# Optimization experiments

Hardware: AMD Instinct MI355X
Metric: run time of the kernel (lower is better)

Reference implementation:

```python
import jax, jax.numpy as jnp
import numpy as np

N, FEAT, D, K, L, H, NCLS = 4096, 512, 64, 100, 3, 8, 2
EPS = 1e-15

def _ln(x, g, b, eps=1e-6):
    m = x.mean(-1, keepdims=True)
    v = x.var(-1, keepdims=True)
    return (x - m) * jax.lax.rsqrt(v + eps) * g + b


def setup_inputs():
    key = jax.random.key(0)
    ks = jax.random.split(key, 12)
    w = lambda k, shape: jax.random.normal(k, shape, jnp.float32) * 0.02
    return {
        "node_feat": jax.random.normal(ks[0], (1, N, FEAT), jnp.float32),
        "adj": jax.random.uniform(ks[1], (1, N, N), jnp.float32),
        "conv_w": w(ks[2], (FEAT, D)), "conv_b": jnp.zeros((D,), jnp.float32),
        "bn_g": jnp.ones((D,), jnp.float32), "bn_b": jnp.zeros((D,), jnp.float32),
        "pool_w": w(ks[3], (D, K)), "pool_b": jnp.zeros((K,), jnp.float32),
        "cls_token": jnp.zeros((1, 1, D), jnp.float32),
        "ln1_g": jnp.ones((L, D), jnp.float32), "ln1_b": jnp.zeros((L, D), jnp.float32),
        "qkv_w": w(ks[4], (L, D, 3 * D)), "qkv_b": jnp.zeros((L, 3 * D), jnp.float32),
        "proj_w": w(ks[5], (L, D, D)), "proj_b": jnp.zeros((L, D), jnp.float32),
        "ln2_g": jnp.ones((L, D), jnp.float32), "ln2_b": jnp.zeros((L, D), jnp.float32),
        "fc1_w": w(ks[6], (L, D, 4 * D)), "fc1_b": jnp.zeros((L, 4 * D), jnp.float32),
        "fc2_w": w(ks[7], (L, 4 * D, D)), "fc2_b": jnp.zeros((L, D), jnp.float32),
        "norm_g": jnp.ones((D,), jnp.float32), "norm_b": jnp.zeros((D,), jnp.float32),
        "head_w": w(ks[8], (D, NCLS)), "head_b": jnp.zeros((NCLS,), jnp.float32),
    }


def _forward(node_feat, adj, conv_w, conv_b, bn_g, bn_b, pool_w, pool_b, cls_token,
             ln1_g, ln1_b, qkv_w, qkv_b, proj_w, proj_b, ln2_g, ln2_b,
             fc1_w, fc1_b, fc2_w, fc2_b, norm_g, norm_b, head_w, head_b):
    x = node_feat  # mask is all ones -> X = mask*X is a no-op
    # --- GCNBlock: propagate + self loop + linear + BatchNorm(train stats) + L2 norm ---
    y = jnp.matmul(adj, x) + x                 # [1,N,F]
    y = y @ conv_w + conv_b                    # [1,N,D]
    m = y.mean(axis=(0, 1))
    v = y.var(axis=(0, 1))
    y = (y - m) * jax.lax.rsqrt(v + 1e-5) * bn_g + bn_b
    y = y / jnp.maximum(jnp.linalg.norm(y, axis=2, keepdims=True), 1e-12)
    # --- cluster assignment ---
    s = jax.nn.softmax(y @ pool_w + pool_b, axis=-1)   # [1,N,K]
    # --- dense_mincut_pool ---
    out = jnp.einsum('bnk,bnd->bkd', s, y)             # [1,K,D]
    sa = s[0].T @ adj[0]                               # [K,N] (the torch.sparse.mm)
    out_adj = (sa @ s[0])[None]                        # [1,K,K]
    mincut_num = jnp.trace(out_adj, axis1=1, axis2=2)  # [1]
    d_flat = adj.sum(-1)                               # [1,N] degrees
    # trace(S^T diag(d) S) = sum_i d_i * ||s_i||^2
    mincut_den = jnp.sum(d_flat[0] * jnp.sum(s[0] ** 2, axis=-1))[None]
    mincut_loss = jnp.mean(-(mincut_num / mincut_den))
    ss = jnp.einsum('bnk,bnl->bkl', s, s)
    i_s = jnp.eye(K, dtype=ss.dtype)
    ortho_loss = jnp.mean(jnp.linalg.norm(
        ss / jnp.linalg.norm(ss, axis=(-1, -2), keepdims=True) - i_s / jnp.linalg.norm(i_s),
        axis=(-1, -2)))
    ind = jnp.arange(K)
    out_adj = out_adj.at[:, ind, ind].set(0.0)
    dd = jnp.sqrt(out_adj.sum(-1))[:, None] + EPS      # [1,1,K]
    out_adj = out_adj / dd / jnp.swapaxes(dd, 1, 2)    # (returned by pool; unused downstream)
    # --- transformer over [cls] + K cluster tokens ---
    t = jnp.concatenate([jnp.broadcast_to(cls_token, (1, 1, D)), out], axis=1)  # [1,K+1,D]
    hd = D // H
    scale = hd ** -0.5
    for l in range(L):
        h = _ln(t, ln1_g[l], ln1_b[l])
        qkv = h @ qkv_w[l] + qkv_b[l]
        q, k, vv = jnp.split(qkv, 3, axis=-1)
        sp = lambda a: a.reshape(1, -1, H, hd).transpose(0, 2, 1, 3)
        q, k, vv = sp(q), sp(k), sp(vv)
        att = jax.nn.softmax(jnp.einsum('bhqd,bhkd->bhqk', q, k) * scale, axis=-1)
        o = jnp.einsum('bhqk,bhkd->bhqd', att, vv).transpose(0, 2, 1, 3).reshape(1, -1, D)
        t = t + (o @ proj_w[l] + proj_b[l])
        h = _ln(t, ln2_g[l], ln2_b[l])
        t = t + (jax.nn.gelu(h @ fc1_w[l] + fc1_b[l], approximate=False) @ fc2_w[l] + fc2_b[l])
    t = _ln(t, norm_g, norm_b)
    logits = t[:, 0] @ head_w + head_b                 # [1,NCLS]
    return logits, mincut_loss, ortho_loss


def reference(node_feat, adj, conv_w, conv_b, bn_g, bn_b, pool_w, pool_b, cls_token,
              ln1_g, ln1_b, qkv_w, qkv_b, proj_w, proj_b, ln2_g, ln2_b,
              fc1_w, fc1_b, fc2_w, fc2_b, norm_g, norm_b, head_w, head_b):
    return _forward(node_feat, adj, conv_w, conv_b, bn_g, bn_b, pool_w, pool_b, cls_token,
                    ln1_g, ln1_b, qkv_w, qkv_b, proj_w, proj_b, ln2_g, ln2_b,
                    fc1_w, fc1_b, fc2_w, fc2_b, norm_g, norm_b, head_w, head_b)
```

## Files before the change

### kernel.cpp

```cpp
#include <hip/hip_runtime.h>
#include <hip/hip_bf16.h>
#include <math.h>

#define NN   4096
#define FEAT 512
#define DIM  64
#define KC   100
#define LL   3

#define OFF_DFLAT   0
#define OFF_CHSUM   4096
#define OFF_CHSQ    4160
#define ZERO_FLOATS 4224
#define OFF_XW      4224
#define OFF_XWPART  (OFF_XW + NN*DIM)
#define OFF_GPART   OFF_XWPART
#define OFF_YPART   (OFF_XWPART + 8*NN*DIM)
#define OFF_Y0      (OFF_YPART + 8*NN*DIM)
#define OFF_TBUF    (OFF_Y0 + NN*DIM)
#define OFF_QKV     (OFF_TBUF + 101*DIM)
#define OFF_SS      (OFF_QKV + 101*192)
#define OFF_DENP    (OFF_SS + KC*KC)
#define OFF_NUMP    (OFF_DENP + 1024)
#define OFF_SB16    (OFF_NUMP + 1024)
#define OFF_STB16   (OFF_SB16 + NN*128/2)
#define OFF_YNT16   (OFF_STB16 + NN*128/2)
#define OFF_XWT16   (OFF_YNT16 + NN*DIM/2)

typedef __attribute__((ext_vector_type(8))) short bfrag;
typedef __attribute__((ext_vector_type(4))) float ffrag;

__device__ __forceinline__ unsigned short f2bf(float f) {
    union { float f; unsigned u; } v; v.f = f;
    return (unsigned short)((v.u + 0x7FFFu + ((v.u >> 16) & 1u)) >> 16);
}
__device__ __forceinline__ float bf2f(unsigned short u) {
    union { unsigned u; float f; } v; v.u = (unsigned)u << 16; return v.f;
}
__device__ __forceinline__ unsigned int pk2(float a, float b) {
    __hip_bfloat162 h = __float22bfloat162_rn(make_float2(a, b));
    return *(unsigned int*)&h;
}

__device__ __forceinline__ float wsum(float v) {
#pragma unroll
    for (int o = 32; o > 0; o >>= 1) v += __shfl_xor(v, o, 64);
    return v;
}
__device__ __forceinline__ float wmax(float v) {
#pragma unroll
    for (int o = 32; o > 0; o >>= 1) v = fmaxf(v, __shfl_xor(v, o, 64));
    return v;
}
__device__ __forceinline__ float hsum32(float v) {
#pragma unroll
    for (int o = 16; o > 0; o >>= 1) v += __shfl_xor(v, o, 64);
    return v;
}
__device__ __forceinline__ float hmax32(float v) {
#pragma unroll
    for (int o = 16; o > 0; o >>= 1) v = fmaxf(v, __shfl_xor(v, o, 64));
    return v;
}

template<int KDIM>
__global__ __launch_bounds__(256) void mm64(const float* __restrict__ A,
                                            const float* __restrict__ B,
                                            float* __restrict__ outp) {
    __shared__ float a_sh[64 * 68];
    __shared__ float b_sh[64 * 68];
    const int t  = threadIdx.x;
    const int rb = blockIdx.x;
    const int kspan = KDIM / gridDim.y;
    const int k0 = blockIdx.y * kspan;
    const int cg = t & 15, rg = t >> 4;
    const int srow = t >> 2, sq = t & 3;
    float4 acc[4];
#pragma unroll
    for (int i = 0; i < 4; ++i) acc[i] = make_float4(0.f, 0.f, 0.f, 0.f);
    const float* arow = A + (size_t)(rb * 64 + srow) * KDIM + k0;
    const float* brow = B + (size_t)(k0 + srow) * DIM;
    for (int kt = 0; kt < kspan; kt += 64) {
#pragma unroll
        for (int k = 0; k < 4; ++k) {
            const int j = sq * 4 + 16 * k;
            *(float4*)&a_sh[srow * 68 + j] = *(const float4*)(arow + kt + j);
            *(float4*)&b_sh[srow * 68 + j] = *(const float4*)(brow + (size_t)kt * DIM + j);
        }
        __syncthreads();
#pragma unroll 4
        for (int jj = 0; jj < 64; jj += 4) {
            const float4 w0 = *(float4*)&b_sh[(jj + 0) * 68 + 4 * cg];
            const float4 w1 = *(float4*)&b_sh[(jj + 1) * 68 + 4 * cg];
            const float4 w2 = *(float4*)&b_sh[(jj + 2) * 68 + 4 * cg];
            const float4 w3 = *(float4*)&b_sh[(jj + 3) * 68 + 4 * cg];
#pragma unroll
            for (int i = 0; i < 4; ++i) {
                const float4 av = *(float4*)&a_sh[(4 * rg + i) * 68 + jj];
                acc[i].x += av.x * w0.x + av.y * w1.x + av.z * w2.x + av.w * w3.x;
                acc[i].y += av.x * w0.y + av.y * w1.y + av.z * w2.y + av.w * w3.y;
                acc[i].z += av.x * w0.z + av.y * w1.z + av.z * w2.z + av.w * w3.z;
                acc[i].w += av.x * w0.w + av.y * w1.w + av.z * w2.w + av.w * w3.w;
            }
        }
        __syncthreads();
    }
    const int M = gridDim.x * 64;
    float* op = outp + (size_t)blockIdx.y * M * DIM;
#pragma unroll
    for (int i = 0; i < 4; ++i)
        *(float4*)&op[(size_t)(rb * 64 + 4 * rg + i) * DIM + 4 * cg] = acc[i];
}

__global__ __launch_bounds__(256) void xwred2(const float* __restrict__ part,
                                              float* __restrict__ xw,
                                              unsigned short* __restrict__ xwT) {
    __shared__ unsigned short tl[64 * 17];
    const int t = threadIdx.x, b = blockIdx.x;
    const int nb = t >> 4, d0 = (t & 15) * 4;
    const size_t e = ((size_t)(b * 16 + nb)) * 64 + d0;
    float4 v = *(const float4*)(part + e);
#pragma unroll
    for (int s = 1; s < 8; ++s) {
        const float4 u = *(const float4*)(part + (size_t)s * NN * DIM + e);
        v.x += u.x; v.y += u.y; v.z += u.z; v.w += u.w;
    }
    *(float4*)(xw + e) = v;
    tl[(d0 + 0) * 17 + nb] = f2bf(v.x);
    tl[(d0 + 1) * 17 + nb] = f2bf(v.y);
    tl[(d0 + 2) * 17 + nb] = f2bf(v.z);
    tl[(d0 + 3) * 17 + nb] = f2bf(v.w);
    __syncthreads();
    const int d = t >> 2, c = (t & 3) * 4;
    ushort4 o;
    o.x = tl[d * 17 + c + 0]; o.y = tl[d * 17 + c + 1];
    o.z = tl[d * 17 + c + 2]; o.w = tl[d * 17 + c + 3];
    *(ushort4*)(xwT + (size_t)d * NN + b * 16 + c) = o;
}

__global__ __launch_bounds__(256) void gemmA(const float* __restrict__ adj,
                                             const unsigned short* __restrict__ xwT,
                                             float* __restrict__ ypart,
                                             float* __restrict__ dflat) {
    __shared__ __align__(16) unsigned short a_sh[32 * 72];
    __shared__ __align__(16) unsigned short b_sh[64 * 72];
    const int t  = threadIdx.x;
    const int rb = blockIdx.x;
    const int k0 = blockIdx.y * 512;
    const int w = t >> 6, lane = t & 63;
    const int m = lane & 15, q = lane >> 4;
    const int ih = w & 1, jh = w >> 1;
    const int srow = t >> 3, sq = t & 7;
    const int bn = t >> 2, bc = t & 3;
    ffrag acc[2];
    acc[0] = (ffrag){0.f, 0.f, 0.f, 0.f};
    acc[1] = (ffrag){0.f, 0.f, 0.f, 0.f};
    float dacc = 0.f;
    const float* abase = adj + (size_t)(rb * 32 + srow) * NN + k0;
    const unsigned short* bbase = xwT + (size_t)bn * NN + k0;
    for (int kt = 0; kt < 512; kt += 64) {
#pragma unroll
        for (int k = 0; k < 2; ++k) {
            const int p = sq + 8 * k;
            const float4 v = *(const float4*)(abase + kt + 4 * p);
            dacc += v.x + v.y + v.z + v.w;
            *(uint2*)(a_sh + srow * 72 + 4 * p) = make_uint2(pk2(v.x, v.y), pk2(v.z, v.w));
        }
#pragma unroll
        for (int k = 0; k < 2; ++k) {
            const int c2 = bc + 4 * k;
            *(bfrag*)(b_sh + bn * 72 + c2 * 8) = *(const bfrag*)(bbase + kt + c2 * 8);
        }
        __syncthreads();
#pragma unroll
        for (int ks = 0; ks < 2; ++ks) {
            const bfrag af = *(const bfrag*)(a_sh + (ih * 16 + m) * 72 + ks * 32 + q * 8);
#pragma unroll
            for (int jj = 0; jj < 2; ++jj) {
                const bfrag bf = *(const bfrag*)(b_sh + ((jh * 2 + jj) * 16 + m) * 72 + ks * 32 + q * 8);
                acc[jj] = __builtin_amdgcn_mfma_f32_16x16x32_bf16(af, bf, acc[jj], 0, 0, 0);
            }
        }
        __syncthreads();
    }
    float* op = ypart + (size_t)blockIdx.y * NN * DIM;
#pragma unroll
    for (int jj = 0; jj < 2; ++jj)
#pragma unroll
        for (int r = 0; r < 4; ++r)
            op[(size_t)(rb * 32 + ih * 16 + q * 4 + r) * DIM + jh * 32 + jj * 16 + m] = acc[jj][r];
    dacc += __shfl_down(dacc, 1, 64);
    dacc += __shfl_down(dacc, 2, 64);
    dacc += __shfl_down(dacc, 4, 64);
    if (sq == 0) atomicAdd(&dflat[rb * 32 + srow], dacc);
}

__global__ __launch_bounds__(256) void spmmT(const float* __restrict__ adj,
                                             const unsigned short* __restrict__ ST,
                                             const unsigned short* __restrict__ Sb16,
                                             float* __restrict__ nump) {
    __shared__ __align__(16) unsigned short a_sh[32 * 72];
    __shared__ __align__(16) unsigned short s_sh[128 * 72];
    __shared__ float red[4];
    const int t  = threadIdx.x;
    const int rb = blockIdx.x;
    const int k0 = blockIdx.y * 512;
    const int w = t >> 6, lane = t & 63;
    const int m = lane & 15, q = lane >> 4;
    const int rh = w & 1, ch = w >> 1;
    const int srow = t >> 3, sq = t & 7;
    const int sn = t >> 1, sc = t & 1;
    ffrag acc[4];
#pragma unroll
    for (int j = 0; j < 4; ++j) acc[j] = (ffrag){0.f, 0.f, 0.f, 0.f};
    const float* abase = adj + (size_t)(rb * 32 + srow) * NN + k0;
    const unsigned short* sbase = ST + (size_t)sn * NN + k0;
    for (int kt = 0; kt < 512; kt += 64) {
#pragma unroll
        for (int k = 0; k < 2; ++k) {
            const int p = sq + 8 * k;
            const float4 v = *(const float4*)(abase + kt + 4 * p);
            *(uint2*)(a_sh + srow * 72 + 4 * p) = make_uint2(pk2(v.x, v.y), pk2(v.z, v.w));
        }
#pragma unroll
        for (int k = 0; k < 4; ++k) {
            const int c2 = sc + 2 * k;
            *(bfrag*)(s_sh + sn * 72 + c2 * 8) = *(const bfrag*)(sbase + kt + c2 * 8);
        }
        __syncthreads();
#pragma unroll
        for (int ks = 0; ks < 2; ++ks) {
            const bfrag af = *(const bfrag*)(a_sh + (rh * 16 + m) * 72 + ks * 32 + q * 8);
#pragma unroll
            for (int j = 0; j < 4; ++j) {
                const bfrag bf = *(const bfrag*)(s_sh + ((ch * 4 + j) * 16 + m) * 72 + ks * 32 + q * 8);
                acc[j] = __builtin_amdgcn_mfma_f32_16x16x32_bf16(af, bf, acc[j], 0, 0, 0);
            }
        }
        __syncthreads();
    }
    float local = 0.f;
#pragma unroll
    for (int j = 0; j < 4; ++j)
#pragma unroll
        for (int r = 0; r < 4; ++r) {
            const int row = rb * 32 + rh * 16 + q * 4 + r;
            const int col = ch * 64 + j * 16 + m;
            local += acc[j][r] * bf2f(Sb16[(size_t)row * 128 + col]);
        }
    local = wsum(local);
    if (lane == 0) red[w] = local;
    __syncthreads();
    if (t == 0) nump[blockIdx.y * 128 + blockIdx.x] = red[0] + red[1] + red[2] + red[3];
}

__global__ __launch_bounds__(256) void bnstat(const float* __restrict__ ypart,
                                              const float* __restrict__ xw,
                                              const float* __restrict__ conv_b,
                                              float* __restrict__ Y0,
                                              float* __restrict__ chsum,
                                              float* __restrict__ chsq) {
    __shared__ float ssum[64], ssq[64];
    const int t = threadIdx.x;
    if (t < 64) { ssum[t] = 0.f; ssq[t] = 0.f; }
    __syncthreads();
    const int tid = blockIdx.x * 256 + t;
    const size_t e = (size_t)tid * 4;
    const int c0 = (int)(e & 63);
    float4 v = *(const float4*)(xw + e);
#pragma unroll
    for (int s = 0; s < 8; ++s) {
        const float4 u = *(const float4*)(ypart + (size_t)s * NN * DIM + e);
        v.x += u.x; v.y += u.y; v.z += u.z; v.w += u.w;
    }
    const float4 b = *(const float4*)(conv_b + c0);
    v.x += b.x; v.y += b.y; v.z += b.z; v.w += b.w;
    *(float4*)(Y0 + e) = v;
    atomicAdd(&ssum[c0 + 0], v.x); atomicAdd(&ssum[c0 + 1], v.y);
    atomicAdd(&ssum[c0 + 2], v.z); atomicAdd(&ssum[c0 + 3], v.w);
    atomicAdd(&ssq[c0 + 0], v.x * v.x); atomicAdd(&ssq[c0 + 1], v.y * v.y);
    atomicAdd(&ssq[c0 + 2], v.z * v.z); atomicAdd(&ssq[c0 + 3], v.w * v.w);
    __syncthreads();
    if (t < 64) { atomicAdd(&chsum[t], ssum[t]); atomicAdd(&chsq[t], ssq[t]); }
}

__global__ __launch_bounds__(256) void rowsk(const float* __restrict__ Y0,
                                             const float* __restrict__ bn_g,
                                             const float* __restrict__ bn_b,
                                             const float* __restrict__ chsum,
                                             const float* __restrict__ chsq,
                                             const float* __restrict__ pool_w,
                                             const float* __restrict__ pool_b,
                                             const float* __restrict__ dflat,
                                             unsigned short* __restrict__ YnT,
                                             unsigned short* __restrict__ Sb16,
                                             float* __restrict__ denp) {
    __shared__ float scale_sh[64], shift_sh[64];
    __shared__ float yn_sh[4][64];
    __shared__ float4 pw4[16 * 104];
    __shared__ float denw[4];
    const int t = threadIdx.x;
    if (t < 64) {
        const float mn  = chsum[t] * (1.f / 4096.f);
        const float var = chsq[t] * (1.f / 4096.f) - mn * mn;
        const float sc  = bn_g[t] * rsqrtf(var + 1e-5f);
        scale_sh[t] = sc;
        shift_sh[t] = bn_b[t] - mn * sc;
    }
    for (int idx = t; idx < 16 * KC; idx += 256) {
        const int dq = idx / KC, k = idx - dq * KC;
        pw4[dq * 104 + k] = make_float4(pool_w[(4 * dq + 0) * KC + k],
                                        pool_w[(4 * dq + 1) * KC + k],
                                        pool_w[(4 * dq + 2) * KC + k],
                                        pool_w[(4 * dq + 3) * KC + k]);
    }
    __syncthreads();
    const int w = t >> 6, lane = t & 63;
    const int row = blockIdx.x * 4 + w;
    float v = Y0[(size_t)row * 64 + lane] * scale_sh[lane] + shift_sh[lane];
    const float nrm = fmaxf(sqrtf(wsum(v * v)), 1e-12f);
    const float yn = v / nrm;
    yn_sh[w][lane] = yn;
    __syncthreads();
    YnT[(size_t)(t >> 2) * NN + blockIdx.x * 4 + (t & 3)] = f2bf(yn_sh[t & 3][t >> 2]);
    const bool v2 = (lane + 64) < KC;
    const int j2 = v2 ? (lane + 64) : 0;
    float L1 = pool_b[lane];
    float L2 = pool_b[j2];
#pragma unroll
    for (int dq = 0; dq < 16; ++dq) {
        const float4 yv = *(const float4*)&yn_sh[w][4 * dq];
        const float4 w1 = pw4[dq * 104 + lane];
        L1 += yv.x * w1.x + yv.y * w1.y + yv.z * w1.z + yv.w * w1.w;
        const float4 w2 = pw4[dq * 104 + j2];
        L2 += yv.x * w2.x + yv.y * w2.y + yv.z * w2.z + yv.w * w2.w;
    }
    const float mx = wmax(fmaxf(L1, v2 ? L2 : -1e30f));
    const float e1 = expf(L1 - mx);
    const float e2 = v2 ? expf(L2 - mx) : 0.f;
    const float inv = 1.f / wsum(e1 + e2);
    const float s1 = e1 * inv, s2 = e2 * inv;
    Sb16[(size_t)row * 128 + lane] = f2bf(s1);
    Sb16[(size_t)row * 128 + 64 + lane] = f2bf(s2);
    const float c = wsum(s1 * s1 + s2 * s2);
    if (lane == 0) denw[w] = dflat[row] * c;
    __syncthreads();
    if (t == 0) denp[blockIdx.x] = denw[0] + denw[1] + denw[2] + denw[3];
}

__global__ __launch_bounds__(256) void transpS(const unsigned short* __restrict__ Sb,
                                               unsigned short* __restrict__ ST) {
    __shared__ __align__(16) unsigned short tl[128 * 72];
    const int t = threadIdx.x, b = blockIdx.x;
#pragma unroll
    for (int p = 0; p < 4; ++p) {
        const int n = (t >> 4) + 16 * p, c = t & 15;
        const bfrag v = *(const bfrag*)(Sb + (size_t)(b * 64 + n) * 128 + c * 8);
        const unsigned short* pv = (const unsigned short*)&v;
#pragma unroll
        for (int u = 0; u < 8; ++u) tl[(c * 8 + u) * 72 + n] = pv[u];
    }
    __syncthreads();
#pragma unroll
    for (int p = 0; p < 4; ++p) {
        const int r = (t >> 3) + 32 * p, c = t & 7;
        *(bfrag*)(ST + (size_t)r * NN + b * 64 + c * 8) = *(const bfrag*)(tl + r * 72 + c * 8);
    }
}

__global__ __launch_bounds__(256) void gram(const unsigned short* __restrict__ ST,
                                            const unsigned short* __restrict__ YnT,
                                            float* __restrict__ gpart) {
    __shared__ __align__(16) unsigned short a_sh[128 * 72];
    __shared__ __align__(16) unsigned short b_sh[192 * 72];
    const int t = threadIdx.x;
    const int k0 = blockIdx.x * 64;
    const int w = t >> 6, lane = t & 63;
    const int m = lane & 15, q = lane >> 4;
#pragma unroll
    for (int p = 0; p < 4; ++p) {
        const int n = (t >> 3) + 32 * p, c = t & 7;
        *(bfrag*)(a_sh + n * 72 + c * 8) = *(const bfrag*)(ST + (size_t)n * NN + k0 + c * 8);
    }
#pragma unroll
    for (int p = 0; p < 6; ++p) {
        const int n = (t >> 3) + 32 * p, c = t & 7;
        const unsigned short* src = (n < 64) ? (YnT + (size_t)n * NN + k0 + c * 8)
                                             : (ST + (size_t)(n - 64) * NN + k0 + c * 8);
        *(bfrag*)(b_sh + n * 72 + c * 8) = *(const bfrag*)src;
    }
    __syncthreads();
    ffrag acc[2][12];
#pragma unroll
    for (int i = 0; i < 2; ++i)
#pragma unroll
        for (int j = 0; j < 12; ++j) acc[i][j] = (ffrag){0.f, 0.f, 0.f, 0.f};
#pragma unroll
    for (int ks = 0; ks < 2; ++ks) {
        const bfrag af0 = *(const bfrag*)(a_sh + (w * 32 +  0 + m) * 72 + ks * 32 + q * 8);
        const bfrag af1 = *(const bfrag*)(a_sh + (w * 32 + 16 + m) * 72 + ks * 32 + q * 8);
#pragma unroll
        for (int j = 0; j < 12; ++j) {
            const bfrag bf = *(const bfrag*)(b_sh + (j * 16 + m) * 72 + ks * 32 + q * 8);
            acc[0][j] = __builtin_amdgcn_mfma_f32_16x16x32_bf16(af0, bf, acc[0][j], 0, 0, 0);
            acc[1][j] = __builtin_amdgcn_mfma_f32_16x16x32_bf16(af1, bf, acc[1][j], 0, 0, 0);
        }
    }
    float* op = gpart + (size_t)blockIdx.x * 128 * 192;
#pragma unroll
    for (int i = 0; i < 2; ++i)
#pragma unroll
        for (int j = 0; j < 12; ++j)
#pragma unroll
            for (int r = 0; r < 4; ++r)
                op[(size_t)(w * 32 + i * 16 + q * 4 + r) * 192 + j * 16 + m] = acc[i][j][r];
}

__global__ __launch_bounds__(256) void gramred(const float* __restrict__ gpart,
                                               const float* __restrict__ cls,
                                               float* __restrict__ tbuf,
                                               float* __restrict__ ss) {
    const int tid = blockIdx.x * 256 + threadIdx.x;
    if (tid < 128 * 192) {
        const int row = tid / 192, col = tid - row * 192;
        float v = 0.f;
        for (int s = 0; s < 64; ++s) v += gpart[(size_t)s * 128 * 192 + tid];
        if (row < KC) {
            if (col < 64) tbuf[(row + 1) * 64 + col] = v;
            else if (col < 164) ss[row * KC + (col - 64)] = v;
        }
    } else if (tid < 128 * 192 + 64) {
        const int c = tid - 128 * 192;
        tbuf[c] = cls[c];
    }
}

__global__ __launch_bounds__(256) void attnA(const float* __restrict__ tbuf,
                                             const float* __restrict__ g1,
                                             const float* __restrict__ b1,
                                             const float* __restrict__ qw,
                                             const float* __restrict__ qb,
                                             float* __restrict__ qkvb, int l) {
    __shared__ float wl[64 * 192];
    __shared__ float hs[64];
    const int t = threadIdx.x, tok = blockIdx.x;
    const float* wsrc = qw + (size_t)l * 64 * 192;
#pragma unroll
    for (int p = 0; p < 12; ++p) {
        const int idx = t + 256 * p;
        *(float4*)&wl[idx * 4] = *(const float4*)(wsrc + idx * 4);
    }
    if (t < 64) {
        const float x = tbuf[tok * 64 + t];
        const float m = wsum(x) * (1.f / 64.f);
        const float var = wsum(x * x) * (1.f / 64.f) - m * m;
        hs[t] = (x - m) * rsqrtf(var + 1e-6f) * g1[l * 64 + t] + b1[l * 64 + t];
    }
    __syncthreads();
    if (t < 192) {
        float a = qb[l * 192 + t];
#pragma unroll 8
        for (int e = 0; e < 64; ++e)
            a += hs[e] * wl[e * 192 + t];
        qkvb[tok * 192 + t] = a;
    }
}

__global__ __launch_bounds__(256) void attnB(float* __restrict__ tbuf,
                                             const float* __restrict__ qkvb,
                                             const float* __restrict__ pw,
                                             const float* __restrict__ pb,
                                             const float* __restrict__ g2,
                                             const float* __restrict__ b2,
                                             const float* __restrict__ w1,
                                             const float* __restrict__ bb1,
                                             const float* __restrict__ w2,
                                             const float* __restrict__ bb2, int l) {
    __shared__ float big[13332];
    __shared__ float sc[8 * 104];
    __shared__ float q_l[64], osh[64], h2sh[64], gsh[256];
    const int t = threadIdx.x, qtok = blockIdx.x;
    float t_old = 0.f;
    if (t < 64) t_old = tbuf[qtok * 64 + t];
#pragma unroll
    for (int p = 0; p < 13; ++p) {
        const int idx = t + 256 * p;
        if (idx < 101 * 32) {
            const int k = idx >> 5, c = idx & 31;
            *(float4*)&big[k * 132 + c * 4] = *(const float4*)(qkvb + k * 192 + 64 + c * 4);
        }
    }
    if (t < 16) *(float4*)&q_l[t * 4] = *(const float4*)(qkvb + qtok * 192 + t * 4);
    __syncthreads();
    const float scale = 0.35355339059327373f;
#pragma unroll
    for (int p = 0; p < 4; ++p) {
        const int idx = t + 256 * p;
        if (idx < 808) {
            const int h = idx / 101, k = idx - h * 101;
            float s = 0.f;
#pragma unroll
            for (int d = 0; d < 8; ++d)
                s += q_l[h * 8 + d] * big[k * 132 + h * 8 + d];
            sc[h * 104 + k] = s * scale;
        }
    }
    __syncthreads();
    {
        const int w = t >> 6;
        const int h = w * 2 + ((t >> 5) & 1);
        const int lft = t & 31;
        float v[4];
#pragma unroll
        for (int g = 0; g < 4; ++g) {
            const int k = lft + 32 * g;
            v[g] = (k < 101) ? sc[h * 104 + k] : -1e30f;
        }
        float m = fmaxf(fmaxf(v[0], v[1]), fmaxf(v[2], v[3]));
        m = hmax32(m);
        float s = 0.f;
#pragma unroll
        for (int g = 0; g < 4; ++g) { v[g] = expf(v[g] - m); s += v[g]; }
        s = hsum32(s);
        const float inv = 1.f / s;
#pragma unroll
        for (int g = 0; g < 4; ++g) {
            const int k = lft + 32 * g;
            if (k < 101) sc[h * 104 + k] = v[g] * inv;
        }
    }
    __syncthreads();
    if (t < 64) {
        const int h = t >> 3, d = t & 7;
        float o = 0.f;
        for (int k = 0; k < 101; ++k)
            o += sc[h * 104 + k] * big[k * 132 + 64 + h * 8 + d];
        osh[h * 8 + d] = o;
    }
    __syncthreads();
#pragma unroll
    for (int p = 0; p < 4; ++p) {
        const int idx = t + 256 * p;
        *(float4*)&big[idx * 4] = *(const float4*)(pw + (size_t)l * 4096 + idx * 4);
    }
    __syncthreads();
    float t1 = 0.f;
    if (t < 64) {
        float pr = pb[l * 64 + t];
#pragma unroll 8
        for (int e = 0; e < 64; ++e)
            pr += osh[e] * big[e * 64 + t];
        t1 = t_old + pr;
        const float m = wsum(t1) * (1.f / 64.f);
        const float var = wsum(t1 * t1) * (1.f / 64.f) - m * m;
        h2sh[t] = (t1 - m) * rsqrtf(var + 1e-6f) * g2[l * 64 + t] + b2[l * 64 + t];
    }
    __syncthreads();
    for (int ch = 0; ch < 2; ++ch) {
#pragma unroll
        for (int p = 0; p < 8; ++p) {
            const int idx = t + 256 * p;
            const int e = idx >> 5, c = idx & 31;
            *(float4*)&big[e * 128 + c * 4] =
                *(const float4*)(w1 + (size_t)l * 16384 + e * 256 + ch * 128 + c * 4);
        }
        __syncthreads();
        if (t < 128) {
            float a = bb1[l * 256 + ch * 128 + t];
#pragma unroll 8
            for (int e = 0; e < 64; ++e)
                a += h2sh[e] * big[e * 128 + t];
            gsh[ch * 128 + t] = 0.5f * a * (1.f + erff(a * 0.70710678118654752f));
        }
        __syncthreads();
    }
    float a2 = (t < 64) ? bb2[l * 64 + t] : 0.f;
    for (int ch = 0; ch < 2; ++ch) {
#pragma unroll
        for (int p = 0; p < 8; ++p) {
            const int idx = t + 256 * p;
            *(float4*)&big[idx * 4] =
                *(const float4*)(w2 + (size_t)l * 16384 + ch * 8192 + idx * 4);
        }
        __syncthreads();
        if (t < 64) {
#pragma unroll 8
            for (int er = 0; er < 128; ++er)
                a2 += gsh[ch * 128 + er] * big[er * 64 + t];
        }
        __syncthreads();
    }
    if (t < 64) tbuf[qtok * 64 + t] = t1 + a2;
}

__global__ __launch_bounds__(256) void finalk(const float* __restrict__ tbuf,
                                              const float* __restrict__ ng,
                                              const float* __restrict__ nb,
                                              const float* __restrict__ hw,
                                              const float* __restrict__ hb,
                                              const float* __restrict__ ss,
                                              const float* __restrict__ denp,
                                              const float* __restrict__ nump,
                                              float* __restrict__ out) {
    __shared__ float f0[64];
    __shared__ float red[256];
    __shared__ float fro_sh, den_sh, num_sh;
    const int t = threadIdx.x;
    if (t < 64) {
        const float x = tbuf[t];
        const float m = wsum(x) * (1.f / 64.f);
        const float var = wsum(x * x) * (1.f / 64.f) - m * m;
        f0[t] = (x - m) * rsqrtf(var + 1e-6f) * ng[t] + nb[t];
    }
    red[t] = denp[t] + denp[t + 256] + denp[t + 512] + denp[t + 768];
    __syncthreads();
    for (int s = 128; s > 0; s >>= 1) { if (t < s) red[t] += red[t + s]; __syncthreads(); }
    if (t == 0) den_sh = red[0];
    __syncthreads();
    red[t] = nump[t] + nump[t + 256] + nump[t + 512] + nump[t + 768];
    __syncthreads();
    for (int s = 128; s > 0; s >>= 1) { if (t < s) red[t] += red[t + s]; __syncthreads(); }
    if (t == 0) num_sh = red[0];
    __syncthreads();
    if (t < 2) {
        float a = hb[t];
        for (int d = 0; d < 64; ++d) a += f0[d] * hw[d * 2 + t];
        out[t] = a;
    }
    if (t == 2) out[2] = -(num_sh / den_sh);
    float s1 = 0.f;
    for (int idx = t; idx < KC * KC; idx += 256) { const float v = ss[idx]; s1 += v * v; }
    __syncthreads();
    red[t] = s1;
    __syncthreads();
    for (int s = 128; s > 0; s >>= 1) { if (t < s) red[t] += red[t + s]; __syncthreads(); }
    if (t == 0) fro_sh = sqrtf(red[0]);
    __syncthreads();
    const float inv = 1.f / fro_sh;
    float s2 = 0.f;
    for (int idx = t; idx < KC * KC; idx += 256) {
        float v = ss[idx] * inv;
        if (idx % 101 == 0) v -= 0.1f;
        s2 += v * v;
    }
    __syncthreads();
    red[t] = s2;
    __syncthreads();
    for (int s = 128; s > 0; s >>= 1) { if (t < s) red[t] += red[t + s]; __syncthreads(); }
    if (t == 0) out[3] = sqrtf(red[0]);
}

extern "C" void kernel_launch(void* const* d_in, const int* in_sizes, int n_in,
                              void* d_out, int out_size, void* d_ws, size_t ws_size,
                              hipStream_t stream) {
    (void)in_sizes; (void)n_in; (void)out_size; (void)ws_size;
    const float* x      = (const float*)d_in[0];
    const float* adj    = (const float*)d_in[1];
    const float* conv_w = (const float*)d_in[2];
    const float* conv_b = (const float*)d_in[3];
    const float* bn_g   = (const float*)d_in[4];
    const float* bn_b   = (const float*)d_in[5];
    const float* pool_w = (const float*)d_in[6];
    const float* pool_b = (const float*)d_in[7];
    const float* cls    = (const float*)d_in[8];
    const float* ln1_g  = (const float*)d_in[9];
    const float* ln1_b  = (const float*)d_in[10];
    const float* qkv_w  = (const float*)d_in[11];
    const float* qkv_b  = (const float*)d_in[12];
    const float* proj_w = (const float*)d_in[13];
    const float* proj_b = (const float*)d_in[14];
    const float* ln2_g  = (const float*)d_in[15];
    const float* ln2_b  = (const float*)d_in[16];
    const float* fc1_w  = (const float*)d_in[17];
    const float* fc1_b  = (const float*)d_in[18];
    const float* fc2_w  = (const float*)d_in[19];
    const float* fc2_b  = (const float*)d_in[20];
    const float* norm_g = (const float*)d_in[21];
    const float* norm_b = (const float*)d_in[22];
    const float* head_w = (const float*)d_in[23];
    const float* head_b = (const float*)d_in[24];
    float* ws  = (float*)d_ws;
    float* out = (float*)d_out;
    unsigned short* Sb16  = (unsigned short*)(ws + OFF_SB16);
    unsigned short* STb16 = (unsigned short*)(ws + OFF_STB16);
    unsigned short* YnT16 = (unsigned short*)(ws + OFF_YNT16);
    unsigned short* xwT16 = (unsigned short*)(ws + OFF_XWT16);

    hipMemsetAsync(ws, 0, ZERO_FLOATS * sizeof(float), stream);
    mm64<FEAT><<<dim3(64, 8), 256, 0, stream>>>(x, conv_w, ws + OFF_XWPART);
    xwred2<<<256, 256, 0, stream>>>(ws + OFF_XWPART, ws + OFF_XW, xwT16);
    gemmA<<<dim3(128, 8), 256, 0, stream>>>(adj, xwT16, ws + OFF_YPART, ws + OFF_DFLAT);
    bnstat<<<256, 256, 0, stream>>>(ws + OFF_YPART, ws + OFF_XW, conv_b,
                                    ws + OFF_Y0, ws + OFF_CHSUM, ws + OFF_CHSQ);
    rowsk<<<1024, 256, 0, stream>>>(ws + OFF_Y0, bn_g, bn_b, ws + OFF_CHSUM, ws + OFF_CHSQ,
                                    pool_w, pool_b, ws + OFF_DFLAT,
                                    YnT16, Sb16, ws + OFF_DENP);
    transpS<<<64, 256, 0, stream>>>(Sb16, STb16);
    spmmT<<<dim3(128, 8), 256, 0, stream>>>(adj, STb16, Sb16, ws + OFF_NUMP);
    gram<<<64, 256, 0, stream>>>(STb16, YnT16, ws + OFF_GPART);
    gramred<<<97, 256, 0, stream>>>(ws + OFF_GPART, cls, ws + OFF_TBUF, ws + OFF_SS);
    for (int l = 0; l < LL; ++l) {
        attnA<<<101, 256, 0, stream>>>(ws + OFF_TBUF, ln1_g, ln1_b, qkv_w, qkv_b, ws + OFF_QKV, l);
        attnB<<<101, 256, 0, stream>>>(ws + OFF_TBUF, ws + OFF_QKV, proj_w, proj_b,
                                       ln2_g, ln2_b, fc1_w, fc1_b, fc2_w, fc2_b, l);
    }
    finalk<<<1, 256, 0, stream>>>(ws + OFF_TBUF, norm_g, norm_b, head_w, head_b,
                                  ws + OFF_SS, ws + OFF_DENP, ws + OFF_NUMP, out);
}
```

Measured before the change: 299.9 us.

## Fuse X·W GEMM with reduction, zeroing, and S transpose into fewer kernels

Replaces the split-K mm64 plus xwred2 pair with a single xwk kernel that computes X·conv_w directly per 16-row tile, writes the fp32 result and bf16 transpose, and zeroes the workspace accumulators (removing hipMemsetAsync). The S transpose kernel is removed by having rowsk write ST directly from shared memory, alongside a restructured YnT write. This cuts three launches and the 8-way partial-sum round trip through memory. In exchange, the xwk GEMM has less parallelism per block, and the transposed writes are narrow 4-element strided stores.

After: 298.4 us. About the same (-0.5%).

```diff
diff --git a/kernel.cpp b/kernel.cpp
--- a/kernel.cpp
+++ b/kernel.cpp
@@ -13,10 +13,9 @@
 #define OFF_CHSQ    4160
 #define ZERO_FLOATS 4224
 #define OFF_XW      4224
-#define OFF_XWPART  (OFF_XW + NN*DIM)
-#define OFF_GPART   OFF_XWPART
-#define OFF_YPART   (OFF_XWPART + 8*NN*DIM)
-#define OFF_Y0      (OFF_YPART + 8*NN*DIM)
+#define OFF_YPART   (OFF_XW + NN*DIM)
+#define OFF_GPART   (OFF_YPART + 8*NN*DIM)
+#define OFF_Y0      (OFF_GPART + 64*128*192)
 #define OFF_TBUF    (OFF_Y0 + NN*DIM)
 #define OFF_QKV     (OFF_TBUF + 101*DIM)
 #define OFF_SS      (OFF_QKV + 101*192)
@@ -63,79 +62,51 @@
     return v;
 }
 
-template<int KDIM>
-__global__ __launch_bounds__(256) void mm64(const float* __restrict__ A,
-                                            const float* __restrict__ B,
-                                            float* __restrict__ outp) {
-    __shared__ float a_sh[64 * 68];
+__global__ __launch_bounds__(256) void xwk(const float* __restrict__ x,
+                                           const float* __restrict__ B,
+                                           float* __restrict__ xw,
+                                           unsigned short* __restrict__ xwT,
+                                           float* __restrict__ zws) {
+    __shared__ float a_sh[16 * 68];
     __shared__ float b_sh[64 * 68];
-    const int t  = threadIdx.x;
-    const int rb = blockIdx.x;
-    const int kspan = KDIM / gridDim.y;
-    const int k0 = blockIdx.y * kspan;
-    const int cg = t & 15, rg = t >> 4;
-    const int srow = t >> 2, sq = t & 3;
-    float4 acc[4];
-#pragma unroll
-    for (int i = 0; i < 4; ++i) acc[i] = make_float4(0.f, 0.f, 0.f, 0.f);
-    const float* arow = A + (size_t)(rb * 64 + srow) * KDIM + k0;
-    const float* brow = B + (size_t)(k0 + srow) * DIM;
-    for (int kt = 0; kt < kspan; kt += 64) {
-#pragma unroll
-        for (int k = 0; k < 4; ++k) {
-            const int j = sq * 4 + 16 * k;
-            *(float4*)&a_sh[srow * 68 + j] = *(const float4*)(arow + kt + j);
-            *(float4*)&b_sh[srow * 68 + j] = *(const float4*)(brow + (size_t)kt * DIM + j);
-        }
-        __syncthreads();
-#pragma unroll 4
-        for (int jj = 0; jj < 64; jj += 4) {
-            const float4 w0 = *(float4*)&b_sh[(jj + 0) * 68 + 4 * cg];
-            const float4 w1 = *(float4*)&b_sh[(jj + 1) * 68 + 4 * cg];
-            const float4 w2 = *(float4*)&b_sh[(jj + 2) * 68 + 4 * cg];
-            const float4 w3 = *(float4*)&b_sh[(jj + 3) * 68 + 4 * cg];
-#pragma unroll
-            for (int i = 0; i < 4; ++i) {
-                const float4 av = *(float4*)&a_sh[(4 * rg + i) * 68 + jj];
-                acc[i].x += av.x * w0.x + av.y * w1.x + av.z * w2.x + av.w * w3.x;
-                acc[i].y += av.x * w0.y + av.y * w1.y + av.z * w2.y + av.w * w3.y;
-                acc[i].z += av.x * w0.z + av.y * w1.z + av.z * w2.z + av.w * w3.z;
-                acc[i].w += av.x * w0.w + av.y * w1.w + av.z * w2.w + av.w * w3.w;
-            }
-        }
-        __syncthreads();
-    }
-    const int M = gridDim.x * 64;
-    float* op = outp + (size_t)blockIdx.y * M * DIM;
-#pragma unroll
-    for (int i = 0; i < 4; ++i)
-        *(float4*)&op[(size_t)(rb * 64 + 4 * rg + i) * DIM + 4 * cg] = acc[i];
-}
-
-__global__ __launch_bounds__(256) void xwred2(const float* __restrict__ part,
-                                              float* __restrict__ xw,
-                                              unsigned short* __restrict__ xwT) {
     __shared__ unsigned short tl[64 * 17];
-    const int t = threadIdx.x, b = blockIdx.x;
-    const int nb = t >> 4, d0 = (t & 15) * 4;
-    const size_t e = ((size_t)(b * 16 + nb)) * 64 + d0;
-    float4 v = *(const float4*)(part + e);
-#pragma unroll
-    for (int s = 1; s < 8; ++s) {
-        const float4 u = *(const float4*)(part + (size_t)s * NN * DIM + e);
-        v.x += u.x; v.y += u.y; v.z += u.z; v.w += u.w;
-    }
-    *(float4*)(xw + e) = v;
-    tl[(d0 + 0) * 17 + nb] = f2bf(v.x);
-    tl[(d0 + 1) * 17 + nb] = f2bf(v.y);
-    tl[(d0 + 2) * 17 + nb] = f2bf(v.z);
-    tl[(d0 + 3) * 17 + nb] = f2bf(v.w);
+    const int t = threadIdx.x, rb = blockIdx.x;
+    if (rb < 17) {
+        const int zi = rb * 256 + t;
+        if (zi < ZERO_FLOATS) zws[zi] = 0.f;
+    }
+    const int r = t >> 4, cg = (t & 15) * 4;
+    float4 acc = make_float4(0.f, 0.f, 0.f, 0.f);
+    for (int kt = 0; kt < FEAT; kt += 64) {
+        *(float4*)&a_sh[(t >> 4) * 68 + (t & 15) * 4] =
+            *(const float4*)(x + (size_t)(rb * 16 + (t >> 4)) * FEAT + kt + (t & 15) * 4);
+#pragma unroll
+        for (int p = 0; p < 4; ++p) {
+            const int idx = t + 256 * p;
+            const int kr = idx >> 4, c4 = (idx & 15) * 4;
+            *(float4*)&b_sh[kr * 68 + c4] = *(const float4*)(B + (size_t)(kt + kr) * DIM + c4);
+        }
+        __syncthreads();
+#pragma unroll 8
+        for (int k = 0; k < 64; ++k) {
+            const float av = a_sh[r * 68 + k];
+            const float4 bv = *(float4*)&b_sh[k * 68 + cg];
+            acc.x += av * bv.x; acc.y += av * bv.y;
+            acc.z += av * bv.z; acc.w += av * bv.w;
+        }
+        __syncthreads();
+    }
+    *(float4*)&xw[(size_t)(rb * 16 + r) * DIM + cg] = acc;
+    tl[(cg + 0) * 17 + r] = f2bf(acc.x);
+    tl[(cg + 1) * 17 + r] = f2bf(acc.y);
+    tl[(cg + 2) * 17 + r] = f2bf(acc.z);
+    tl[(cg + 3) * 17 + r] = f2bf(acc.w);
     __syncthreads();
     const int d = t >> 2, c = (t & 3) * 4;
     ushort4 o;
     o.x = tl[d * 17 + c + 0]; o.y = tl[d * 17 + c + 1];
     o.z = tl[d * 17 + c + 2]; o.w = tl[d * 17 + c + 3];
-    *(ushort4*)(xwT + (size_t)d * NN + b * 16 + c) = o;
+    *(ushort4*)(xwT + (size_t)d * NN + rb * 16 + c) = o;
 }
 
 __global__ __launch_bounds__(256) void gemmA(const float* __restrict__ adj,
@@ -209,7 +180,7 @@
     const int m = lane & 15, q = lane >> 4;
     const int rh = w & 1, ch = w >> 1;
     const int srow = t >> 3, sq = t & 7;
-    const int sn = t >> 1, sc = t & 1;
+    const int sn = t >> 1, sc2 = t & 1;
     ffrag acc[4];
 #pragma unroll
     for (int j = 0; j < 4; ++j) acc[j] = (ffrag){0.f, 0.f, 0.f, 0.f};
@@ -224,7 +195,7 @@
         }
 #pragma unroll
         for (int k = 0; k < 4; ++k) {
-            const int c2 = sc + 2 * k;
+            const int c2 = sc2 + 2 * k;
             *(bfrag*)(s_sh + sn * 72 + c2 * 8) = *(const bfrag*)(sbase + kt + c2 * 8);
         }
         __syncthreads();
@@ -294,10 +265,12 @@
                                              const float* __restrict__ dflat,
                                              unsigned short* __restrict__ YnT,
                                              unsigned short* __restrict__ Sb16,
+                                             unsigned short* __restrict__ ST,
                                              float* __restrict__ denp) {
     __shared__ float scale_sh[64], shift_sh[64];
     __shared__ float yn_sh[4][64];
     __shared__ float4 pw4[16 * 104];
+    __shared__ unsigned short sb_sh[4][128];
     __shared__ float denw[4];
     const int t = threadIdx.x;
     if (t < 64) {
@@ -321,12 +294,11 @@
     const float nrm = fmaxf(sqrtf(wsum(v * v)), 1e-12f);
     const float yn = v / nrm;
     yn_sh[w][lane] = yn;
-    __syncthreads();
-    YnT[(size_t)(t >> 2) * NN + blockIdx.x * 4 + (t & 3)] = f2bf(yn_sh[t & 3][t >> 2]);
     const bool v2 = (lane + 64) < KC;
     const int j2 = v2 ? (lane + 64) : 0;
     float L1 = pool_b[lane];
     float L2 = pool_b[j2];
+    __syncthreads();
 #pragma unroll
     for (int dq = 0; dq < 16; ++dq) {
         const float4 yv = *(const float4*)&yn_sh[w][4 * dq];
@@ -340,31 +312,27 @@
     const float e2 = v2 ? expf(L2 - mx) : 0.f;
     const float inv = 1.f / wsum(e1 + e2);
     const float s1 = e1 * inv, s2 = e2 * inv;
-    Sb16[(size_t)row * 128 + lane] = f2bf(s1);
-    Sb16[(size_t)row * 128 + 64 + lane] = f2bf(s2);
+    const unsigned short b1 = f2bf(s1), b2 = f2bf(s2);
+    Sb16[(size_t)row * 128 + lane] = b1;
+    Sb16[(size_t)row * 128 + 64 + lane] = b2;
+    sb_sh[w][lane] = b1;
+    sb_sh[w][64 + lane] = b2;
     const float c = wsum(s1 * s1 + s2 * s2);
     if (lane == 0) denw[w] = dflat[row] * c;
     __syncthreads();
-    if (t == 0) denp[blockIdx.x] = denw[0] + denw[1] + denw[2] + denw[3];
-}
-
-__global__ __launch_bounds__(256) void transpS(const unsigned short* __restrict__ Sb,
-                                               unsigned short* __restrict__ ST) {
-    __shared__ __align__(16) unsigned short tl[128 * 72];
-    const int t = threadIdx.x, b = blockIdx.x;
-#pragma unroll
-    for (int p = 0; p < 4; ++p) {
-        const int n = (t >> 4) + 16 * p, c = t & 15;
-        const bfrag v = *(const bfrag*)(Sb + (size_t)(b * 64 + n) * 128 + c * 8);
-        const unsigned short* pv = (const unsigned short*)&v;
-#pragma unroll
-        for (int u = 0; u < 8; ++u) tl[(c * 8 + u) * 72 + n] = pv[u];
-    }
-    __syncthreads();
-#pragma unroll
-    for (int p = 0; p < 4; ++p) {
-        const int r = (t >> 3) + 32 * p, c = t & 7;
-        *(bfrag*)(ST + (size_t)r * NN + b * 64 + c * 8) = *(const bfrag*)(tl + r * 72 + c * 8);
+    if (t < 64) {
+        ushort4 o;
+        o.x = f2bf(yn_sh[0][t]); o.y = f2bf(yn_sh[1][t]);
+        o.z = f2bf(yn_sh[2][t]); o.w = f2bf(yn_sh[3][t]);
+        *(ushort4*)(YnT + (size_t)t * NN + blockIdx.x * 4) = o;
+    } else if (t < 192) {
+        const int c2 = t - 64;
+        ushort4 o;
+        o.x = sb_sh[0][c2]; o.y = sb_sh[1][c2];
+        o.z = sb_sh[2][c2]; o.w = sb_sh[3][c2];
+        *(ushort4*)(ST + (size_t)c2 * NN + blockIdx.x * 4) = o;
+    } else if (t == 192) {
+        denp[blockIdx.x] = denw[0] + denw[1] + denw[2] + denw[3];
     }
 }
 
@@ -686,16 +654,13 @@
     unsigned short* YnT16 = (unsigned short*)(ws + OFF_YNT16);
     unsigned short* xwT16 = (unsigned short*)(ws + OFF_XWT16);
 
-    hipMemsetAsync(ws, 0, ZERO_FLOATS * sizeof(float), stream);
-    mm64<FEAT><<<dim3(64, 8), 256, 0, stream>>>(x, conv_w, ws + OFF_XWPART);
-    xwred2<<<256, 256, 0, stream>>>(ws + OFF_XWPART, ws + OFF_XW, xwT16);
+    xwk<<<256, 256, 0, stream>>>(x, conv_w, ws + OFF_XW, xwT16, ws);
     gemmA<<<dim3(128, 8), 256, 0, stream>>>(adj, xwT16, ws + OFF_YPART, ws + OFF_DFLAT);
     bnstat<<<256, 256, 0, stream>>>(ws + OFF_YPART, ws + OFF_XW, conv_b,
                                     ws + OFF_Y0, ws + OFF_CHSUM, ws + OFF_CHSQ);
     rowsk<<<1024, 256, 0, stream>>>(ws + OFF_Y0, bn_g, bn_b, ws + OFF_CHSUM, ws + OFF_CHSQ,
                                     pool_w, pool_b, ws + OFF_DFLAT,
-                                    YnT16, Sb16, ws + OFF_DENP);
-    transpS<<<64, 256, 0, stream>>>(Sb16, STb16);
+                                    YnT16, Sb16, STb16, ws + OFF_DENP);
     spmmT<<<dim3(128, 8), 256, 0, stream>>>(adj, STb16, Sb16, ws + OFF_NUMP);
     gram<<<64, 256, 0, stream>>>(STb16, YnT16, ws + OFF_GPART);
     gramred<<<97, 256, 0, stream>>>(ws + OFF_GPART, cls, ws + OFF_TBUF, ws + OFF_SS);
```
